# Performance work log

Measured on AMD Instinct MI355X. Metric: run time of the kernel, lower is better.

Reference implementation:

```python
import jax, jax.numpy as jnp
import numpy as np

B, T, DIM = 1, 2048, 2048
H, KV, D = 16, 4, 128
REP = H // KV
L, S = 32, 16          # cmp_len, cmp_stride
LP = 64                # slc_block
TOPK = 16
WIN = 512
CMP_HID = 2 * D
GATE_HID = DIM // 4
SCALE = D ** -0.5
TC = (T - L) // S + 1  # number of compressed blocks
NS = T // LP           # number of selection blocks
NEG = -1e30


def setup_inputs() -> dict:
    key = jax.random.key(0)
    ks = jax.random.split(key, 12)
    n = lambda k, sh: jax.random.normal(k, sh, jnp.float32) * 0.02
    return dict(
        x=jax.random.normal(ks[0], (B, T, DIM), jnp.float32),
        W_qkv=n(ks[1], ((H + 2 * KV) * D, DIM)), b_qkv=jnp.zeros(((H + 2 * KV) * D,), jnp.float32),
        W_out=n(ks[2], (DIM, H * D)), b_out=jnp.zeros((DIM,), jnp.float32),
        sinks=jnp.zeros((H,), jnp.float32),
        cmp_pos=n(ks[3], (L, D)),
        W_c1=n(ks[4], (CMP_HID, L * D)), b_c1=jnp.zeros((CMP_HID,), jnp.float32),
        W_c2=n(ks[5], (D, CMP_HID)), b_c2=jnp.zeros((D,), jnp.float32),
        W_g1=n(ks[6], (GATE_HID, DIM)), b_g1=jnp.zeros((GATE_HID,), jnp.float32),
        W_g2=n(ks[7], (3, GATE_HID)), b_g2=jnp.array([-2.2, -2.2, 1.4], jnp.float32),
    )


def _nsa(x, W_qkv, b_qkv, W_out, b_out, sinks, cmp_pos,
         W_c1, b_c1, W_c2, b_c2, W_g1, b_g1, W_g2, b_g2):
    qkv = x @ W_qkv.T + b_qkv
    q = qkv[..., :H * D].reshape(B, T, H, D)
    k = qkv[..., H * D:(H + KV) * D].reshape(B, T, KV, D)
    v = qkv[..., (H + KV) * D:].reshape(B, T, KV, D)

    t_idx = jnp.arange(T)
    # ---- compression phi over overlapping blocks (Eq 7) ----
    starts = jnp.arange(TC) * S
    gidx = starts[:, None] + jnp.arange(L)[None, :]          # [TC,L]

    def compress(z):                                          # [B,T,KV,D] -> [B,TC,KV,D]
        blk = z[:, gidx] + cmp_pos[None, None, :, None, :]    # [B,TC,L,KV,D]
        blk = blk.transpose(0, 1, 3, 2, 4).reshape(B, TC, KV, L * D)
        h = jax.nn.gelu(blk @ W_c1.T + b_c1, approximate=False)
        return h @ W_c2.T + b_c2

    k_cmp = jnp.repeat(compress(k), REP, axis=2)              # [B,TC,H,D]
    v_cmp = jnp.repeat(compress(v), REP, axis=2)

    # ---- CMP attention (Eq 8) ----
    c_logits = jnp.einsum('bthd,bchd->bhtc', q, k_cmp) * SCALE
    valid = (starts[None, :] + L - 1) <= t_idx[:, None]       # block fully in past [T,TC]
    c_logits = jnp.where(valid[None, None], c_logits, NEG)
    p = jax.nn.softmax(c_logits, axis=-1)
    any_valid = valid.any(axis=-1)                            # [T]
    p = jnp.where(any_valid[None, None, :, None], p, 0.0)
    o_cmp = jnp.einsum('bhtc,bchd->bthd', p, v_cmp)

    # ---- block score aggregation (Eq 9) + head sum (Eq 10) ----
    j_idx = jnp.arange(NS)
    ov = (starts[None, :] < (j_idx[:, None] + 1) * LP) & (starts[None, :] + L > j_idx[:, None] * LP)
    blk_scores = jnp.einsum('bhtc,jc->btj', p, ov.astype(p.dtype))  # [B,T,NS]
    cur_blk = t_idx // LP
    masked = jnp.where((j_idx[None, :] >= cur_blk[:, None])[None], -jnp.inf, blk_scores)
    _, dyn_idx = jax.lax.top_k(masked, TOPK - 3)              # Eq 11 (3 fixed blocks)
    fixed = jnp.stack([jnp.zeros_like(cur_blk), jnp.clip(cur_blk - 2, 0),
                       jnp.clip(cur_blk - 1, 0)], axis=-1)    # [T,3]
    all_blk = jnp.concatenate([jnp.broadcast_to(fixed[None], (B, T, 3)), dyn_idx], axis=-1)

    # ---- SLC sparse block attention (Eq 12) ----
    allowed = jax.nn.one_hot(all_blk, NS).sum(-2) > 0         # [B,T,NS]
    allowed = allowed | (j_idx[None, None, :] == cur_blk[None, :, None])  # own block dense
    tok_allowed = jnp.repeat(allowed, LP, axis=-1)            # [B,T,T]
    causal = t_idx[None, :] <= t_idx[:, None]                 # [T,T] (query, key)
    K = jnp.repeat(k, REP, axis=2)
    V = jnp.repeat(v, REP, axis=2)
    base = jnp.einsum('bthd,bshd->bhts', q, K) * SCALE        # shared logits
    s_logits = jnp.where((tok_allowed & causal[None])[:, None], base, NEG)
    o_slc = jnp.einsum('bhts,bshd->bthd', jax.nn.softmax(s_logits, -1), V)

    # ---- SWA sliding window with attention sinks ----
    swa_mask = causal & (t_idx[None, :] > t_idx[:, None] - WIN)
    w_logits = jnp.where(swa_mask[None, None], base, NEG)
    sink = jnp.broadcast_to(sinks[None, :, None, None], (B, H, T, 1))
    pw = jax.nn.softmax(jnp.concatenate([w_logits, sink], axis=-1), -1)[..., :T]
    o_swa = jnp.einsum('bhts,bshd->bthd', pw, V)

    # ---- sigmoid gating (Eq 5) + output proj ----
    g = jax.nn.sigmoid(jax.nn.gelu(x @ W_g1.T + b_g1, approximate=False) @ W_g2.T + b_g2)
    o = (g[..., 0, None, None] * o_cmp + g[..., 1, None, None] * o_slc
         + g[..., 2, None, None] * o_swa)                     # [B,T,H,D]
    return o.reshape(B, T, H * D) @ W_out.T + b_out


def reference(x, W_qkv, b_qkv, W_out, b_out, sinks, cmp_pos,
              W_c1, b_c1, W_c2, b_c2, W_g1, b_g1, W_g2, b_g2):
    return _nsa(x, W_qkv, b_qkv, W_out, b_out, sinks, cmp_pos,
                W_c1, b_c1, W_c2, b_c2, W_g1, b_g1, W_g2, b_g2)
```

## Files before the change

### kernel.cpp

```cpp
#include <hip/hip_runtime.h>
#include <hip/hip_bf16.h>

#define DEV static __device__ __forceinline__

constexpr int T_ = 2048, DIM_ = 2048, H_ = 16, KVH = 4, D_ = 128;
constexpr int LL = 32, SS = 16, TOPK_ = 16, WIN_ = 512;
constexpr int GATE_HID_ = 512;
constexpr int TC_ = 127, NS_ = 32;
constexpr int QKV_N = (H_ + 2 * KVH) * D_;
constexpr float SCALE_ = 0.08838834764831845f;

typedef __attribute__((ext_vector_type(8))) short short8;
typedef __attribute__((ext_vector_type(4))) float f32x4;
typedef __attribute__((ext_vector_type(4))) float float4v;
typedef __attribute__((ext_vector_type(4))) unsigned short u16x4;

DEV unsigned short f2b(float x) {
    return __builtin_bit_cast(unsigned short, __float2bfloat16(x));
}
DEV float b2f(unsigned short u) { return __builtin_bit_cast(float, ((unsigned)u) << 16); }
DEV float gelu_f(float x) { return 0.5f * x * (1.f + erff(x * 0.70710678118654752f)); }

DEV void g2l16(const void* g, void* l) {
    __builtin_amdgcn_global_load_lds((const __attribute__((address_space(1))) unsigned int*)g,
                                     (__attribute__((address_space(3))) unsigned int*)l, 16, 0, 0);
}

__global__ void cvt_f2b(const float* __restrict__ s, unsigned short* __restrict__ d, int n) {
    const int i = (blockIdx.x * 256 + threadIdx.x) * 4;
    if (i >= n) return;
    float4v v = *(const float4v*)(s + i);
    u16x4 o;
#pragma unroll
    for (int j = 0; j < 4; j++) o[j] = f2b(v[j]);
    *(u16x4*)(d + i) = o;
}

__global__ void cvt_all(const float* __restrict__ x, const float* __restrict__ wq,
                        const float* __restrict__ wg, const float* __restrict__ wc1,
                        const float* __restrict__ wc2,
                        unsigned short* __restrict__ xb, unsigned short* __restrict__ wqb,
                        unsigned short* __restrict__ wgb, unsigned short* __restrict__ wc1b,
                        unsigned short* __restrict__ wc2b) {
    const long i = ((long)blockIdx.x * 256 + threadIdx.x) * 4;
    const float* s;
    unsigned short* d;
    long off;
    if (i < 4194304)        { s = x;   d = xb;   off = i; }
    else if (i < 10485760)  { s = wq;  d = wqb;  off = i - 4194304; }
    else if (i < 11534336)  { s = wg;  d = wgb;  off = i - 10485760; }
    else if (i < 12582912)  { s = wc1; d = wc1b; off = i - 11534336; }
    else if (i < 12615680)  { s = wc2; d = wc2b; off = i - 12582912; }
    else return;
    float4v v = *(const float4v*)(s + off);
    u16x4 o;
#pragma unroll
    for (int j = 0; j < 4; j++) o[j] = f2b(v[j]);
    *(u16x4*)(d + off) = o;
}

DEV void stage64(const unsigned short* __restrict__ src, unsigned short* dstL,
                 int K, int tid) {
#pragma unroll
    for (int it = 0; it < 4; it++) {
        const int e = it * 256 + tid;
        const int row = e >> 3, cg = e & 7;
        g2l16(src + (size_t)row * K + ((cg ^ (row & 7)) << 3), dstL + e * 8);
    }
}
DEV short8 frag64(const unsigned short* Ls, int row, int g) {
    return *(const short8*)&Ls[row * 64 + ((g ^ (row & 7)) << 3)];
}

template <int ACT, bool WF, bool WB>
__global__ __launch_bounds__(256) void gemm_f(const unsigned short* __restrict__ A,
                                              const unsigned short* __restrict__ B,
                                              const float* __restrict__ bias,
                                              float* __restrict__ Cf,
                                              unsigned short* __restrict__ Cb,
                                              int M, int N, int K) {
    __shared__ __align__(16) unsigned short As[128 * 64];
    __shared__ __align__(16) unsigned short Bs[128 * 64];
    const int tid = threadIdx.x;
    const int w = tid >> 6, l = tid & 63;
    const int lc = l & 15, lg = l >> 4;
    const int wr = w >> 1, wc = w & 1;
    const int m0 = blockIdx.y * 128, n0 = blockIdx.x * 128;
    f32x4 acc[4][4] = {};
    for (int k0 = 0; k0 < K; k0 += 64) {
        stage64(A + (size_t)m0 * K + k0, As, K, tid);
        stage64(B + (size_t)n0 * K + k0, Bs, K, tid);
        __syncthreads();
#pragma unroll
        for (int ks = 0; ks < 2; ks++) {
            short8 af[4], bfr[4];
#pragma unroll
            for (int mi = 0; mi < 4; mi++) af[mi] = frag64(As, wr * 64 + mi * 16 + lc, ks * 4 + lg);
#pragma unroll
            for (int ni = 0; ni < 4; ni++) bfr[ni] = frag64(Bs, wc * 64 + ni * 16 + lc, ks * 4 + lg);
#pragma unroll
            for (int mi = 0; mi < 4; mi++)
#pragma unroll
                for (int ni = 0; ni < 4; ni++)
                    acc[mi][ni] = __builtin_amdgcn_mfma_f32_16x16x32_bf16(af[mi], bfr[ni], acc[mi][ni], 0, 0, 0);
        }
        __syncthreads();
    }
#pragma unroll
    for (int mi = 0; mi < 4; mi++) {
        const int gr = m0 + wr * 64 + mi * 16 + lg * 4;
#pragma unroll
        for (int ni = 0; ni < 4; ni++) {
            const int gc = n0 + wc * 64 + ni * 16 + lc;
            const float bv = bias[gc];
#pragma unroll
            for (int r = 0; r < 4; r++) {
                float v = acc[mi][ni][r] + bv;
                if (ACT == 1) v = gelu_f(v);
                const size_t idx = (size_t)(gr + r) * N + gc;
                if (WF) Cf[idx] = v;
                if (WB) Cb[idx] = f2b(v);
            }
        }
    }
}

__global__ __launch_bounds__(256) void gemm_qkvg(const unsigned short* __restrict__ A,
                                                 const unsigned short* __restrict__ Bq,
                                                 const unsigned short* __restrict__ Bg,
                                                 const float* __restrict__ bq,
                                                 const float* __restrict__ bg,
                                                 unsigned short* __restrict__ Cq,
                                                 float* __restrict__ Cg) {
    __shared__ __align__(16) unsigned short As[128 * 64];
    __shared__ __align__(16) unsigned short Bs[128 * 64];
    const int K = DIM_;
    const int tid = threadIdx.x;
    const int w = tid >> 6, l = tid & 63;
    const int lc = l & 15, lg = l >> 4;
    const int wr = w >> 1, wc = w & 1;
    const int m0 = blockIdx.y * 128, n0 = blockIdx.x * 128;
    const bool isg = (n0 >= QKV_N);
    const unsigned short* B = isg ? (Bg + (size_t)(n0 - QKV_N) * K) : (Bq + (size_t)n0 * K);
    f32x4 acc[4][4] = {};
    for (int k0 = 0; k0 < K; k0 += 64) {
        stage64(A + (size_t)m0 * K + k0, As, K, tid);
        stage64(B + k0, Bs, K, tid);
        __syncthreads();
#pragma unroll
        for (int ks = 0; ks < 2; ks++) {
            short8 af[4], bfr[4];
#pragma unroll
            for (int mi = 0; mi < 4; mi++) af[mi] = frag64(As, wr * 64 + mi * 16 + lc, ks * 4 + lg);
#pragma unroll
            for (int ni = 0; ni < 4; ni++) bfr[ni] = frag64(Bs, wc * 64 + ni * 16 + lc, ks * 4 + lg);
#pragma unroll
            for (int mi = 0; mi < 4; mi++)
#pragma unroll
                for (int ni = 0; ni < 4; ni++)
                    acc[mi][ni] = __builtin_amdgcn_mfma_f32_16x16x32_bf16(af[mi], bfr[ni], acc[mi][ni], 0, 0, 0);
        }
        __syncthreads();
    }
#pragma unroll
    for (int mi = 0; mi < 4; mi++) {
        const int gr = m0 + wr * 64 + mi * 16 + lg * 4;
#pragma unroll
        for (int ni = 0; ni < 4; ni++) {
            const int gcl = (n0 - (isg ? QKV_N : 0)) + wc * 64 + ni * 16 + lc;
            const float bv = isg ? bg[gcl] : bq[gcl];
#pragma unroll
            for (int r = 0; r < 4; r++) {
                const float v = acc[mi][ni][r] + bv;
                if (isg) Cg[(size_t)(gr + r) * GATE_HID_ + gcl] = gelu_f(v);
                else Cq[(size_t)(gr + r) * QKV_N + gcl] = f2b(v);
            }
        }
    }
}

__global__ __launch_bounds__(256) void gemm_c1p(const unsigned short* __restrict__ A,
                                                const unsigned short* __restrict__ B,
                                                float* __restrict__ part) {
    __shared__ __align__(16) unsigned short As[128 * 64];
    __shared__ __align__(16) unsigned short Bs[128 * 64];
    const int K = 4096, N = 256;
    const int tid = threadIdx.x;
    const int w = tid >> 6, l = tid & 63;
    const int lc = l & 15, lg = l >> 4;
    const int wr = w >> 1, wc = w & 1;
    const int m0 = blockIdx.y * 128, n0 = blockIdx.x * 128;
    const int kz = blockIdx.z * 1024;
    f32x4 acc[4][4] = {};
    for (int k0 = kz; k0 < kz + 1024; k0 += 64) {
        stage64(A + (size_t)m0 * K + k0, As, K, tid);
        stage64(B + (size_t)n0 * K + k0, Bs, K, tid);
        __syncthreads();
#pragma unroll
        for (int ks = 0; ks < 2; ks++) {
            short8 af[4], bfr[4];
#pragma unroll
            for (int mi = 0; mi < 4; mi++) af[mi] = frag64(As, wr * 64 + mi * 16 + lc, ks * 4 + lg);
#pragma unroll
            for (int ni = 0; ni < 4; ni++) bfr[ni] = frag64(Bs, wc * 64 + ni * 16 + lc, ks * 4 + lg);
#pragma unroll
            for (int mi = 0; mi < 4; mi++)
#pragma unroll
                for (int ni = 0; ni < 4; ni++)
                    acc[mi][ni] = __builtin_amdgcn_mfma_f32_16x16x32_bf16(af[mi], bfr[ni], acc[mi][ni], 0, 0, 0);
        }
        __syncthreads();
    }
    float* dst = part + (size_t)blockIdx.z * 2048 * 256;
#pragma unroll
    for (int mi = 0; mi < 4; mi++) {
        const int gr = m0 + wr * 64 + mi * 16 + lg * 4;
#pragma unroll
        for (int ni = 0; ni < 4; ni++) {
            const int gc = n0 + wc * 64 + ni * 16 + lc;
#pragma unroll
            for (int r = 0; r < 4; r++) dst[(size_t)(gr + r) * N + gc] = acc[mi][ni][r];
        }
    }
}

__global__ void c1_red(const float* __restrict__ part, const float* __restrict__ bias,
                       unsigned short* __restrict__ out) {
    const int i4 = blockIdx.x * 256 + threadIdx.x;
    const int base = i4 * 4;
    const int col = base & 255;
    float4v v = *(const float4v*)(part + base);
#pragma unroll
    for (int z = 1; z < 4; z++) {
        float4v p = *(const float4v*)(part + (size_t)z * 524288 + base);
#pragma unroll
        for (int j = 0; j < 4; j++) v[j] += p[j];
    }
    u16x4 o;
#pragma unroll
    for (int j = 0; j < 4; j++) o[j] = f2b(gelu_f(v[j] + bias[col + j]));
    *(u16x4*)(out + base) = o;
}

__global__ __launch_bounds__(256) void gemm_c2(const unsigned short* __restrict__ A,
                                               const unsigned short* __restrict__ B,
                                               const float* __restrict__ bias,
                                               unsigned short* __restrict__ Cb,
                                               unsigned short* __restrict__ vcmpT) {
    __shared__ __align__(16) unsigned short As[128 * 64];
    __shared__ __align__(16) unsigned short Bs[128 * 64];
    const int K = 256, N = 128;
    const int tid = threadIdx.x;
    const int w = tid >> 6, l = tid & 63;
    const int lc = l & 15, lg = l >> 4;
    const int wr = w >> 1, wc = w & 1;
    const int m0 = blockIdx.y * 128;
    f32x4 acc[4][4] = {};
    for (int k0 = 0; k0 < K; k0 += 64) {
        stage64(A + (size_t)m0 * K + k0, As, K, tid);
        stage64(B + k0, Bs, K, tid);
        __syncthreads();
#pragma unroll
        for (int ks = 0; ks < 2; ks++) {
            short8 af[4], bfr[4];
#pragma unroll
            for (int mi = 0; mi < 4; mi++) af[mi] = frag64(As, wr * 64 + mi * 16 + lc, ks * 4 + lg);
#pragma unroll
            for (int ni = 0; ni < 4; ni++) bfr[ni] = frag64(Bs, wc * 64 + ni * 16 + lc, ks * 4 + lg);
#pragma unroll
            for (int mi = 0; mi < 4; mi++)
#pragma unroll
                for (int ni = 0; ni < 4; ni++)
                    acc[mi][ni] = __builtin_amdgcn_mfma_f32_16x16x32_bf16(af[mi], bfr[ni], acc[mi][ni], 0, 0, 0);
        }
        __syncthreads();
    }
#pragma unroll
    for (int mi = 0; mi < 4; mi++) {
        const int gr = m0 + wr * 64 + mi * 16 + lg * 4;
#pragma unroll
        for (int ni = 0; ni < 4; ni++) {
            const int gc = wc * 64 + ni * 16 + lc;
            const float bv = bias[gc];
#pragma unroll
            for (int r = 0; r < 4; r++) {
                const int row = gr + r;
                const float v = acc[mi][ni][r] + bv;
                const unsigned short bv16 = f2b(v);
                Cb[(size_t)row * N + gc] = bv16;
                if (row >= 1024) {
                    const int mm = row - 1024;
                    const int cc = mm >> 2, kvv = mm & 3;
                    if (cc < 128) vcmpT[((size_t)(kvv * 128 + gc)) * 128 + cc] = bv16;
                }
            }
        }
    }
}

__global__ __launch_bounds__(256) void post_qkv(const unsigned short* __restrict__ qkvb,
                                                const float* __restrict__ cmp_pos,
                                                const float* __restrict__ hg,
                                                const float* __restrict__ Wg2,
                                                const float* __restrict__ bg2,
                                                unsigned short* __restrict__ kvTs,
                                                float* __restrict__ gate,
                                                unsigned short* __restrict__ blk) {
    const int bb = blockIdx.x;
    const int tid = threadIdx.x;
    if (bb < 128) {
        const int kv = bb & 3, tb = bb >> 2;
        const int t0 = tb * 64;
        unsigned short* dstK = kvTs + (size_t)(kv * 32 + tb) * 16384;
        unsigned short* dstV = dstK + 8192;
        const int kcol0 = H_ * D_ + kv * D_;
        const int vcol0 = H_ * D_ + KVH * D_ + kv * D_;
#pragma unroll
        for (int it = 0; it < 4; it++) {
            const int c = it * 256 + tid;
            const int key = c >> 4, g = c & 15;
            short8 v = *(const short8*)(qkvb + (size_t)(t0 + key) * QKV_N + kcol0 + g * 8);
            *(short8*)(dstK + key * 128 + ((g ^ (key & 7)) << 3)) = v;
        }
        __shared__ __align__(16) unsigned short tile[64][136];
        const int rr = tid >> 4, d0 = (tid & 15) * 8;
#pragma unroll
        for (int mIt = 0; mIt < 4; mIt++) {
            const int row = rr + mIt * 16;
            *(short8*)&tile[row][d0] = *(const short8*)(qkvb + (size_t)(t0 + row) * QKV_N + vcol0 + d0);
        }
        __syncthreads();
        const int d = tid >> 1, half = tid & 1;
        unsigned short* dv = dstV + d * 64;
#pragma unroll
        for (int c2 = 0; c2 < 4; c2++) {
            const int g = half * 4 + c2;
            short8 v;
#pragma unroll
            for (int j = 0; j < 8; j++) v[j] = tile[g * 8 + j][d];
            *(short8*)(dv + ((g ^ (d & 7)) << 3)) = v;
        }
    } else if (bb < 1664) {
        const int gi = (bb - 128) * 4 + (tid >> 6);
        const int t = gi / 3, i = gi % 3;
        const int l = tid & 63;
        const float* h = hg + (size_t)t * GATE_HID_;
        const float* w = Wg2 + (size_t)i * GATE_HID_;
        float s = 0.f;
#pragma unroll
        for (int j = 0; j < GATE_HID_ / 64; j++) s += h[l + j * 64] * w[l + j * 64];
#pragma unroll
        for (int o = 32; o > 0; o >>= 1) s += __shfl_xor(s, o);
        if (l == 0) gate[gi] = 1.f / (1.f + expf(-(s + bg2[i])));
    } else {
        const int b = bb - 1664;
        const int which = b >> 10, m = b & 1023;
        unsigned short* dst = blk + ((size_t)(which * 1024 + m)) * (LL * D_);
        if (m >= TC_ * KVH) {
            short8 z = {};
#pragma unroll
            for (int it = 0; it < 2; it++) *(short8*)(dst + (tid + it * 256) * 8) = z;
            return;
        }
        const int c = m >> 2, kv = m & 3;
        const int col0 = H_ * D_ + which * KVH * D_ + kv * D_;
#pragma unroll
        for (int it = 0; it < 2; it++) {
            const int g = tid + it * 256;
            const int lrow = g >> 4, d0 = (g & 15) * 8;
            short8 z = *(const short8*)(qkvb + (size_t)(c * SS + lrow) * QKV_N + col0 + d0);
            float4v p0 = *(const float4v*)(cmp_pos + lrow * 128 + d0);
            float4v p1 = *(const float4v*)(cmp_pos + lrow * 128 + d0 + 4);
            short8 o;
#pragma unroll
            for (int j = 0; j < 4; j++) o[j] = (short)f2b(b2f((unsigned short)z[j]) + p0[j]);
#pragma unroll
            for (int j = 0; j < 4; j++) o[4 + j] = (short)f2b(b2f((unsigned short)z[4 + j]) + p1[j]);
            *(short8*)(dst + g * 8) = o;
        }
    }
}

__global__ __launch_bounds__(256) void cmp_attn2(const unsigned short* __restrict__ qkvb,
                                                 const unsigned short* __restrict__ kcmpb,
                                                 const unsigned short* __restrict__ vcmpT,
                                                 const float* __restrict__ gate,
                                                 float* __restrict__ obuf,
                                                 float* __restrict__ scg) {
    const int bid = blockIdx.x;
    const int kv = bid & 3;
    const int tx = bid >> 2;
    const int tt = (tx & 1) ? (tx >> 1) : (127 - (tx >> 1));
    const int t0 = tt * 16;
    const int tid = threadIdx.x;
    const int w = tid >> 6, l = tid & 63;
    const int lc = l & 15, lg = l >> 4;
    const int h = kv * 4 + w;

    __shared__ float pbuf[4][16][132];

    short8 aq[4];
    {
        const unsigned short* qp = qkvb + (size_t)(t0 + lc) * QKV_N + h * D_ + lg * 8;
#pragma unroll
        for (int ks = 0; ks < 4; ks++) aq[ks] = *(const short8*)(qp + ks * 32);
    }

    f32x4 sfr[8] = {};
#pragma unroll
    for (int nj = 0; nj < 8; nj++) {
        const int c = nj * 16 + lc;
        const unsigned short* kp = kcmpb + ((size_t)(c * 4 + kv)) * D_ + lg * 8;
#pragma unroll
        for (int ks = 0; ks < 4; ks++) {
            short8 bf = *(const short8*)(kp + ks * 32);
            sfr[nj] = __builtin_amdgcn_mfma_f32_16x16x32_bf16(aq[ks], bf, sfr[nj], 0, 0, 0);
        }
    }

#pragma unroll
    for (int r = 0; r < 4; r++) {
        const int t = t0 + lg * 4 + r;
        const int nv = (t >= LL - 1) ? ((t - (LL - 1)) >> 4) + 1 : 0;
        float lv[8], mx = -1e30f;
#pragma unroll
        for (int nj = 0; nj < 8; nj++) {
            const int c = nj * 16 + lc;
            const float v = (c < nv) ? sfr[nj][r] * SCALE_ : -1e30f;
            lv[nj] = v;
            mx = fmaxf(mx, v);
        }
#pragma unroll
        for (int o = 1; o < 16; o <<= 1) mx = fmaxf(mx, __shfl_xor(mx, o));
        float s = 0.f, pe[8];
#pragma unroll
        for (int nj = 0; nj < 8; nj++) {
            const float e = (lv[nj] > -1e29f) ? __expf(lv[nj] - mx) : 0.f;
            pe[nj] = e;
            s += e;
        }
#pragma unroll
        for (int o = 1; o < 16; o <<= 1) s += __shfl_xor(s, o);
        const float inv = (s > 0.f) ? 1.f / s : 0.f;
#pragma unroll
        for (int nj = 0; nj < 8; nj++) sfr[nj][r] = pe[nj] * inv;
    }

#pragma unroll
    for (int nj = 0; nj < 8; nj++)
#pragma unroll
        for (int r = 0; r < 4; r++) pbuf[w][lg * 4 + r][nj * 16 + lc] = sfr[nj][r];

    __syncthreads();

    for (int idx = tid; idx < 16 * NS_; idx += 256) {
        const int lt = idx >> 5, j = idx & 31;
        int clo = 4 * j - 1;
        if (clo < 0) clo = 0;
        const int chi = 4 * j + 3;
        float s = 0.f;
        for (int c = clo; c <= chi; c++)
            s += pbuf[0][lt][c] + pbuf[1][lt][c] + pbuf[2][lt][c] + pbuf[3][lt][c];
        scg[((size_t)kv * T_ + (t0 + lt)) * NS_ + j] = s;
    }

    short8 pa[4];
#pragma unroll
    for (int ks = 0; ks < 4; ks++) {
        const float* pr = &pbuf[w][lc][ks * 32 + lg * 8];
        short8 t;
#pragma unroll
        for (int j = 0; j < 8; j++) t[j] = (short)f2b(pr[j]);
        pa[ks] = t;
    }
    f32x4 acc[8] = {};
#pragma unroll
    for (int nj = 0; nj < 8; nj++) {
        const int dd = nj * 16 + lc;
        const unsigned short* vp = vcmpT + ((size_t)(kv * 128 + dd)) * 128 + lg * 8;
#pragma unroll
        for (int ks = 0; ks < 4; ks++) {
            short8 bf = *(const short8*)(vp + ks * 32);
            acc[nj] = __builtin_amdgcn_mfma_f32_16x16x32_bf16(pa[ks], bf, acc[nj], 0, 0, 0);
        }
    }

#pragma unroll
    for (int r = 0; r < 4; r++) {
        const int t = t0 + lg * 4 + r;
        const float g0 = gate[t * 3 + 0];
#pragma unroll
        for (int nj = 0; nj < 8; nj++)
            obuf[(size_t)t * (H_ * D_) + h * D_ + nj * 16 + lc] = g0 * acc[nj][r];
    }
}

__global__ __launch_bounds__(256) void topk_k(const float* __restrict__ scg,
                                              unsigned int* __restrict__ amask) {
    const int t = blockIdx.x * 256 + threadIdx.x;
    if (t >= T_) return;
    float sc[NS_];
#pragma unroll
    for (int j = 0; j < NS_; j++)
        sc[j] = scg[((size_t)0 * T_ + t) * NS_ + j] + scg[((size_t)1 * T_ + t) * NS_ + j] +
                scg[((size_t)2 * T_ + t) * NS_ + j] + scg[((size_t)3 * T_ + t) * NS_ + j];
    const int cur = t >> 6;
    unsigned int chosen = 0;
    for (int it = 0; it < TOPK_ - 3; it++) {
        float best = 0.f;
        int bj = -1;
        for (int j = 0; j < NS_; j++) {
            if ((chosen >> j) & 1u) continue;
            const float v = (j >= cur) ? -INFINITY : sc[j];
            if (bj < 0 || v > best) { best = v; bj = j; }
        }
        chosen |= 1u << bj;
    }
    int f1 = cur - 2; if (f1 < 0) f1 = 0;
    int f2 = cur - 1; if (f2 < 0) f2 = 0;
    chosen |= 1u | (1u << f1) | (1u << f2) | (1u << cur);
    amask[t] = chosen;
}

DEV void write_P(unsigned short* PsW, const float p[4][4], int lc, int lg) {
#pragma unroll
    for (int kt = 0; kt < 4; kt++) {
        const int col = kt * 16 + lc;
#pragma unroll
        for (int rp = 0; rp < 4; rp += 2) {
            unsigned int pk;
            asm("v_cvt_pk_bf16_f32 %0, %1, %2" : "=v"(pk) : "v"(p[kt][rp]), "v"(p[kt][rp + 1]));
            const int row0 = lg * 4 + rp;
            const int row1 = row0 + 1;
            PsW[row0 * 64 + (col ^ ((row0 & 7) << 3))] = (unsigned short)(pk & 0xFFFFu);
            PsW[row1 * 64 + (col ^ ((row1 & 7) << 3))] = (unsigned short)(pk >> 16);
        }
    }
}

DEV void stageKV(const unsigned short* __restrict__ src, unsigned short* dst, int tid) {
#pragma unroll
    for (int it = 0; it < 8; it++) {
        const int c = it * 256 + tid;
        g2l16(src + c * 8, dst + c * 8);
    }
}

__global__ __launch_bounds__(256) void slc_swa_pt(const unsigned short* __restrict__ qkvb,
                                                  const unsigned short* __restrict__ kvTs,
                                                  const unsigned int* __restrict__ amask,
                                                  float* __restrict__ mlp,
                                                  unsigned short* __restrict__ accp) {
    const int bid = blockIdx.x;
    const int pr = bid >> 5;
    const int hs = bid & 31;
    const int h = hs >> 1, seg = hs & 1;
    const int kv = h >> 2;
    const int tid = threadIdx.x;
    const int w = tid >> 6, l = tid & 63;
    const int lc = l & 15, lg = l >> 4;

    __shared__ __align__(16) unsigned short KV[2][16384];
    __shared__ __align__(16) unsigned short Ps[4][1024];

    const short8 ones = {0x3F80, 0x3F80, 0x3F80, 0x3F80, 0x3F80, 0x3F80, 0x3F80, 0x3F80};

    for (int it2 = 0; it2 < 2; it2++) {
        const int qb = it2 ? pr : (31 - pr);
        const int t0 = qb * 64;
        const int cur = qb;

        const unsigned int aml = amask[t0 + l];
        unsigned int u64v = aml;
#pragma unroll
        for (int o = 1; o < 64; o <<= 1) u64v |= __shfl_xor(u64v, o);
        unsigned int u16g = aml;
#pragma unroll
        for (int o = 1; o < 16; o <<= 1) u16g |= __shfl_xor(u16g, o);
        const unsigned int uni16 = __shfl(u16g, w * 16);
        unsigned int amr[4];
        int tq[4];
#pragma unroll
        for (int r = 0; r < 4; r++) {
            const int rl = w * 16 + lg * 4 + r;
            tq[r] = t0 + rl;
            amr[r] = __shfl(aml, rl);
        }
        const int tmin_w = t0 + w * 16;
        const int tmax_w = tmin_w + 15;

        const unsigned int curm = (cur >= 31) ? 0xFFFFFFFFu : ((1u << (cur + 1)) - 1u);
        int sl = qb - 8; if (sl < 0) sl = 0;
        const unsigned int swab = curm & ~((1u << sl) - 1u);
        const unsigned int act = (u64v & curm) | swab;
        unsigned int actseg = 0;
        {
            int rank = 0;
            for (int jb = 0; jb <= cur; jb++)
                if ((act >> jb) & 1u) {
                    if ((rank & 1) == seg) actseg |= 1u << jb;
                    rank++;
                }
        }

        short8 aq[4];
        {
            const unsigned short* qp = qkvb + (size_t)(t0 + w * 16 + lc) * QKV_N + h * D_ + lg * 8;
#pragma unroll
            for (int ks = 0; ks < 4; ks++) aq[ks] = *(const short8*)(qp + ks * 32);
        }

        f32x4 acc_s[8] = {};
        f32x4 acc_w[8] = {};
        f32x4 ls4 = {}, lw4 = {};
        float m[4];
#pragma unroll
        for (int r = 0; r < 4; r++) m[r] = -1e30f;

        const unsigned short* kvbase = kvTs + (size_t)kv * 32 * 16384;

        unsigned int rem = actseg;
        if (rem) {
            int jb = __ffs(rem) - 1;
            rem &= rem - 1;
            stageKV(kvbase + (size_t)jb * 16384, KV[0], tid);
            __syncthreads();
            int buf = 0;
            while (true) {
                const int jn = rem ? (__ffs(rem) - 1) : -1;
                if (jn >= 0) {
                    rem &= rem - 1;
                    stageKV(kvbase + (size_t)jn * 16384, KV[buf ^ 1], tid);
                }
                const bool slc_w = (uni16 >> jb) & 1u;
                const bool swa_w = (jb * 64 + 63) > (tmin_w - WIN_);
                if (slc_w || swa_w) {
                    const unsigned short* Kb = KV[buf];
                    const unsigned short* Vb = KV[buf] + 8192;
                    f32x4 sfr[4] = {};
                    __builtin_amdgcn_s_setprio(1);
#pragma unroll
                    for (int kt = 0; kt < 4; kt++) {
                        const int key = kt * 16 + lc;
#pragma unroll
                        for (int ks = 0; ks < 4; ks++) {
                            short8 bf = *(const short8*)&Kb[key * 128 + (((ks * 4 + lg) ^ (key & 7)) << 3)];
                            sfr[kt] = __builtin_amdgcn_mfma_f32_16x16x32_bf16(aq[ks], bf, sfr[kt], 0, 0, 0);
                        }
                    }
                    __builtin_amdgcn_s_setprio(0);
                    float base[4][4];
#pragma unroll
                    for (int kt = 0; kt < 4; kt++)
#pragma unroll
                        for (int r = 0; r < 4; r++) base[kt][r] = sfr[kt][r] * SCALE_;

                    float lmax[4];
#pragma unroll
                    for (int r = 0; r < 4; r++)
                        lmax[r] = fmaxf(fmaxf(base[0][r], base[1][r]), fmaxf(base[2][r], base[3][r]));
                    bool need = false;
#pragma unroll
                    for (int r = 0; r < 4; r++) need |= (lmax[r] > m[r] + 8.f);
                    if (__any(need)) {
#pragma unroll
                        for (int r = 0; r < 4; r++) {
                            float rm = lmax[r];
#pragma unroll
                            for (int o = 1; o < 16; o <<= 1) rm = fmaxf(rm, __shfl_xor(rm, o));
                            const float mn = fmaxf(m[r], rm);
                            const float scf = __expf(m[r] - mn);
                            m[r] = mn;
#pragma unroll
                            for (int j = 0; j < 8; j++) { acc_s[j][r] *= scf; acc_w[j][r] *= scf; }
                            ls4[r] *= scf;
                            lw4[r] *= scf;
                        }
                    }
                    float e[4][4];
#pragma unroll
                    for (int kt = 0; kt < 4; kt++)
#pragma unroll
                        for (int r = 0; r < 4; r++) e[kt][r] = __expf(base[kt][r] - m[r]);

                    if (slc_w) {
                        float ps[4][4];
                        if (jb < cur) {
                            float mr[4];
#pragma unroll
                            for (int r = 0; r < 4; r++) mr[r] = (float)((amr[r] >> jb) & 1u);
#pragma unroll
                            for (int kt = 0; kt < 4; kt++)
#pragma unroll
                                for (int r = 0; r < 4; r++) ps[kt][r] = e[kt][r] * mr[r];
                        } else {
#pragma unroll
                            for (int kt = 0; kt < 4; kt++) {
                                const int kpos = jb * 64 + kt * 16 + lc;
#pragma unroll
                                for (int r = 0; r < 4; r++) {
                                    const bool ok = (kpos <= tq[r]) && ((amr[r] >> jb) & 1u);
                                    ps[kt][r] = ok ? e[kt][r] : 0.f;
                                }
                            }
                        }
                        write_P(Ps[w], ps, lc, lg);
                        __builtin_amdgcn_s_setprio(1);
#pragma unroll
                        for (int ks2 = 0; ks2 < 2; ks2++) {
                            short8 af = *(const short8*)&Ps[w][lc * 64 + ((ks2 * 32 + lg * 8) ^ ((lc & 7) << 3))];
                            ls4 = __builtin_amdgcn_mfma_f32_16x16x32_bf16(af, ones, ls4, 0, 0, 0);
#pragma unroll
                            for (int nj = 0; nj < 8; nj++) {
                                const int dd = nj * 16 + lc;
                                short8 bf = *(const short8*)&Vb[dd * 64 + (((ks2 * 4 + lg) ^ (dd & 7)) << 3)];
                                acc_s[nj] = __builtin_amdgcn_mfma_f32_16x16x32_bf16(af, bf, acc_s[nj], 0, 0, 0);
                            }
                        }
                        __builtin_amdgcn_s_setprio(0);
                    }
                    if (swa_w) {
                        const bool fullwin = (jb < cur) && (jb * 64 > tmax_w - WIN_);
                        if (fullwin) {
                            write_P(Ps[w], e, lc, lg);
                        } else {
                            float pw[4][4];
#pragma unroll
                            for (int kt = 0; kt < 4; kt++) {
                                const int kpos = jb * 64 + kt * 16 + lc;
#pragma unroll
                                for (int r = 0; r < 4; r++) {
                                    const bool ok = (kpos <= tq[r]) && (kpos > tq[r] - WIN_);
                                    pw[kt][r] = ok ? e[kt][r] : 0.f;
                                }
                            }
                            write_P(Ps[w], pw, lc, lg);
                        }
                        __builtin_amdgcn_s_setprio(1);
#pragma unroll
                        for (int ks2 = 0; ks2 < 2; ks2++) {
                            short8 af = *(const short8*)&Ps[w][lc * 64 + ((ks2 * 32 + lg * 8) ^ ((lc & 7) << 3))];
                            lw4 = __builtin_amdgcn_mfma_f32_16x16x32_bf16(af, ones, lw4, 0, 0, 0);
#pragma unroll
                            for (int nj = 0; nj < 8; nj++) {
                                const int dd = nj * 16 + lc;
                                short8 bf = *(const short8*)&Vb[dd * 64 + (((ks2 * 4 + lg) ^ (dd & 7)) << 3)];
                                acc_w[nj] = __builtin_amdgcn_mfma_f32_16x16x32_bf16(af, bf, acc_w[nj], 0, 0, 0);
                            }
                        }
                        __builtin_amdgcn_s_setprio(0);
                    }
                }
                __syncthreads();
                buf ^= 1;
                if (jn < 0) break;
                jb = jn;
            }
        }

        const size_t base2 = (size_t)(qb * 16 + h) * 2 + seg;
        if (lc == 0) {
#pragma unroll
            for (int r = 0; r < 4; r++) {
                const int row = w * 16 + lg * 4 + r;
                float4v v;
                v[0] = m[r]; v[1] = ls4[r]; v[2] = m[r]; v[3] = lw4[r];
                *(float4v*)&mlp[(base2 * 64 + row) * 4] = v;
            }
        }
#pragma unroll
        for (int st = 0; st < 2; st++) {
            const f32x4* A = st ? acc_w : acc_s;
#pragma unroll
            for (int nj = 0; nj < 8; nj++)
#pragma unroll
                for (int r = 0; r < 4; r++) {
                    const int row = w * 16 + lg * 4 + r;
                    accp[((base2 * 2 + st) * 64 + row) * 128 + nj * 16 + lc] = f2b(A[nj][r]);
                }
        }
    }
}

__global__ __launch_bounds__(256) void slc_comb(const float* __restrict__ obuf,
                                                const float* __restrict__ mlp,
                                                const unsigned short* __restrict__ accp,
                                                const float* __restrict__ gate,
                                                const float* __restrict__ sinks,
                                                unsigned short* __restrict__ obufb) {
    const int t = blockIdx.x;
    const int qb = t >> 6, row = t & 63;
    const int tid = threadIdx.x;
    const int d = tid & 127, half = tid >> 7;
    const float g1 = gate[t * 3 + 1], g2 = gate[t * 3 + 2];
#pragma unroll
    for (int hh = 0; hh < 8; hh++) {
        const int h = half * 8 + hh;
        const size_t base2 = (size_t)(qb * 16 + h) * 2;
        const float4v ml0 = *(const float4v*)&mlp[((base2 + 0) * 64 + row) * 4];
        const float4v ml1 = *(const float4v*)&mlp[((base2 + 1) * 64 + row) * 4];
        const float Ms = fmaxf(ml0[0], ml1[0]);
        const float e0 = __expf(ml0[0] - Ms), e1 = __expf(ml1[0] - Ms);
        const float ls = ml0[1] * e0 + ml1[1] * e1;
        const float a0 = b2f(accp[(((base2 + 0) * 2 + 0) * 64 + row) * 128 + d]);
        const float a1 = b2f(accp[(((base2 + 1) * 2 + 0) * 64 + row) * 128 + d]);
        const float os = (a0 * e0 + a1 * e1) / ls;
        const float snk = sinks[h];
        const float Mw = fmaxf(fmaxf(ml0[2], ml1[2]), snk);
        const float w0 = __expf(ml0[2] - Mw), w1 = __expf(ml1[2] - Mw);
        const float den = ml0[3] * w0 + ml1[3] * w1 + __expf(snk - Mw);
        const float b0 = b2f(accp[(((base2 + 0) * 2 + 1) * 64 + row) * 128 + d]);
        const float b1 = b2f(accp[(((base2 + 1) * 2 + 1) * 64 + row) * 128 + d]);
        const float ow = (b0 * w0 + b1 * w1) / den;
        const size_t idx = (size_t)t * (H_ * D_) + h * D_ + d;
        obufb[idx] = f2b(obuf[idx] + g1 * os + g2 * ow);
    }
}

extern "C" void kernel_launch(void* const* d_in, const int* in_sizes, int n_in,
                              void* d_out, int out_size, void* d_ws, size_t ws_size,
                              hipStream_t stream) {
    const float* x = (const float*)d_in[0];
    const float* W_qkv = (const float*)d_in[1];
    const float* b_qkv = (const float*)d_in[2];
    const float* W_out = (const float*)d_in[3];
    const float* b_out = (const float*)d_in[4];
    const float* sinks = (const float*)d_in[5];
    const float* cmp_pos = (const float*)d_in[6];
    const float* W_c1 = (const float*)d_in[7];
    const float* b_c1 = (const float*)d_in[8];
    const float* W_c2 = (const float*)d_in[9];
    const float* b_c2 = (const float*)d_in[10];
    const float* W_g1 = (const float*)d_in[11];
    const float* b_g1 = (const float*)d_in[12];
    const float* W_g2 = (const float*)d_in[13];
    const float* b_g2 = (const float*)d_in[14];

    char* ws = (char*)d_ws;
    unsigned short* qkvb = (unsigned short*)(ws + 0);
    unsigned short* obufb = (unsigned short*)(ws + 0);
    char* A0 = ws + 12582912;
    unsigned short* Wqkv_b = (unsigned short*)(A0);
    unsigned short* blkb = (unsigned short*)(A0);
    float* obuf = (float*)(A0);
    char* B0 = ws + 29360128;
    unsigned short* x_b = (unsigned short*)(B0);
    unsigned short* kvTs = (unsigned short*)(B0);
    float* gateb = (float*)(ws + 37748736);
    unsigned int* amaskb = (unsigned int*)(ws + 37773312);
    float* scg = (float*)(ws + 37781504);
    float* mlp = (float*)(ws + 38830080);
    unsigned short* accp = (unsigned short*)(ws + 39878656);
    unsigned short* Wg1_b = (unsigned short*)(ws + 39878656);
    unsigned short* Wc1_b = (unsigned short*)(ws + 41975808);
    unsigned short* Wc2_b = (unsigned short*)(ws + 44072960);
    float* hgate = (float*)(ws + 44138496);
    unsigned short* hc_b = (unsigned short*)(ws + 48332800);
    unsigned short* hcmpb = (unsigned short*)(ws + 49381376);
    unsigned short* vcmpT = (unsigned short*)(ws + 49905664);
    float* c1part = (float*)(ws + 50036736);
    unsigned short* Wout_b = (unsigned short*)(ws + 39878656);
    float* outf = (float*)d_out;

    cvt_all<<<dim3(12320), 256, 0, stream>>>(x, W_qkv, W_g1, W_c1, W_c2,
                                             x_b, Wqkv_b, Wg1_b, Wc1_b, Wc2_b);
    gemm_qkvg<<<dim3((QKV_N + GATE_HID_) / 128, T_ / 128), 256, 0, stream>>>(
        x_b, Wqkv_b, Wg1_b, b_qkv, b_g1, qkvb, hgate);
    post_qkv<<<dim3(3712), 256, 0, stream>>>(qkvb, cmp_pos, hgate, W_g2, b_g2,
                                             kvTs, gateb, blkb);
    gemm_c1p<<<dim3(2, 16, 4), 256, 0, stream>>>(blkb, Wc1_b, c1part);
    c1_red<<<dim3(512), 256, 0, stream>>>(c1part, b_c1, hc_b);
    gemm_c2<<<dim3(1, 16), 256, 0, stream>>>(hc_b, Wc2_b, b_c2, hcmpb, vcmpT);
    cmp_attn2<<<dim3(512), 256, 0, stream>>>(qkvb, hcmpb, vcmpT, gateb, obuf, scg);
    topk_k<<<dim3(T_ / 256), 256, 0, stream>>>(scg, amaskb);
    slc_swa_pt<<<dim3(512), 256, 0, stream>>>(qkvb, kvTs, amaskb, mlp, accp);
    slc_comb<<<dim3(T_), 256, 0, stream>>>(obuf, mlp, accp, gateb, sinks, obufb);
    cvt_f2b<<<dim3(4096), 256, 0, stream>>>(W_out, Wout_b, DIM_ * H_ * D_);
    gemm_f<0, true, false><<<dim3(DIM_ / 128, T_ / 128), 256, 0, stream>>>(
        obufb, Wout_b, b_out, outf, nullptr, T_, DIM_, H_ * D_);
}
```

Baseline: 314.0 us.

## Split slc_swa work across key halves and row halves, launch 4x more blocks

Reworks the selection/sliding-window attention kernel so that each block handles 32 query rows instead of two 64-row passes. The four waves split as two row tiles times two key halves of each KV block, and the two key halves' softmax partial states are merged through shared memory at the end. The KV double buffer becomes a single buffer, which cuts LDS use so four blocks can fit per CU under launch_bounds(256,4), and the grid grows from 512 to 2048 blocks. The aim is more parallelism and occupancy. In exchange the kernel loses the overlap from prefetching the next KV block, stages the same KV blocks more times in total, and pays for an extra cross-wave reduction.

```diff
diff --git a/kernel.cpp b/kernel.cpp
--- a/kernel.cpp
+++ b/kernel.cpp
@@ -522,263 +522,284 @@
     amask[t] = chosen;
 }
 
-DEV void write_P(unsigned short* PsW, const float p[4][4], int lc, int lg) {
-#pragma unroll
-    for (int kt = 0; kt < 4; kt++) {
+DEV void stageKV(const unsigned short* __restrict__ src, unsigned short* dst, int tid) {
+#pragma unroll
+    for (int it = 0; it < 8; it++) {
+        const int c = it * 256 + tid;
+        g2l16(src + c * 8, dst + c * 8);
+    }
+}
+
+DEV void write_P2(unsigned short* PsW, const float p[2][4], int lc, int lg) {
+#pragma unroll
+    for (int kt = 0; kt < 2; kt++) {
         const int col = kt * 16 + lc;
+        const int gsw = (((col >> 3)) << 3);
 #pragma unroll
         for (int rp = 0; rp < 4; rp += 2) {
             unsigned int pk;
             asm("v_cvt_pk_bf16_f32 %0, %1, %2" : "=v"(pk) : "v"(p[kt][rp]), "v"(p[kt][rp + 1]));
             const int row0 = lg * 4 + rp;
             const int row1 = row0 + 1;
-            PsW[row0 * 64 + (col ^ ((row0 & 7) << 3))] = (unsigned short)(pk & 0xFFFFu);
-            PsW[row1 * 64 + (col ^ ((row1 & 7) << 3))] = (unsigned short)(pk >> 16);
-        }
-    }
-}
-
-DEV void stageKV(const unsigned short* __restrict__ src, unsigned short* dst, int tid) {
-#pragma unroll
-    for (int it = 0; it < 8; it++) {
-        const int c = it * 256 + tid;
-        g2l16(src + c * 8, dst + c * 8);
-    }
-}
-
-__global__ __launch_bounds__(256) void slc_swa_pt(const unsigned short* __restrict__ qkvb,
-                                                  const unsigned short* __restrict__ kvTs,
-                                                  const unsigned int* __restrict__ amask,
-                                                  float* __restrict__ mlp,
-                                                  unsigned short* __restrict__ accp) {
+            const int c0 = ((((col >> 3) ^ (row0 & 3)) << 3) | (col & 7));
+            const int c1 = ((((col >> 3) ^ (row1 & 3)) << 3) | (col & 7));
+            PsW[row0 * 32 + c0] = (unsigned short)(pk & 0xFFFFu);
+            PsW[row1 * 32 + c1] = (unsigned short)(pk >> 16);
+        }
+    }
+}
+
+__global__ __launch_bounds__(256, 4) void slc_swa_pt(const unsigned short* __restrict__ qkvb,
+                                                     const unsigned short* __restrict__ kvTs,
+                                                     const unsigned int* __restrict__ amask,
+                                                     float* __restrict__ mlp,
+                                                     unsigned short* __restrict__ accp) {
     const int bid = blockIdx.x;
-    const int pr = bid >> 5;
-    const int hs = bid & 31;
-    const int h = hs >> 1, seg = hs & 1;
+    const int qb = 31 - (bid >> 6);
+    const int rest = bid & 63;
+    const int h = rest >> 2;
+    const int rh = (rest >> 1) & 1;
+    const int seg = rest & 1;
     const int kv = h >> 2;
     const int tid = threadIdx.x;
     const int w = tid >> 6, l = tid & 63;
     const int lc = l & 15, lg = l >> 4;
-
-    __shared__ __align__(16) unsigned short KV[2][16384];
-    __shared__ __align__(16) unsigned short Ps[4][1024];
+    const int rt = w & 1, kh = w >> 1;
+    const int cur = qb;
+    const int tbase = qb * 64 + rh * 32;
+
+    __shared__ __align__(16) unsigned short KV[16384];
+    __shared__ __align__(16) unsigned short Ps[4][512];
+    __shared__ float mml[2][16][4];
+
+    const unsigned int aml = amask[tbase + (l & 31)];
+    unsigned int u32v = aml;
+#pragma unroll
+    for (int o = 1; o < 64; o <<= 1) u32v |= __shfl_xor(u32v, o);
+    unsigned int um = (((l & 31) >> 4) == rt) ? aml : 0u;
+#pragma unroll
+    for (int o = 1; o < 64; o <<= 1) um |= __shfl_xor(um, o);
+    const unsigned int uni16 = um;
+    unsigned int amr[4];
+#pragma unroll
+    for (int r = 0; r < 4; r++) amr[r] = __shfl(aml, rt * 16 + lg * 4 + r);
+    const int tmin_w = tbase + rt * 16;
+    const int tmax_w = tmin_w + 15;
+
+    const unsigned int curm = (cur >= 31) ? 0xFFFFFFFFu : ((1u << (cur + 1)) - 1u);
+    int sl = qb - 8; if (sl < 0) sl = 0;
+    const unsigned int swab = curm & ~((1u << sl) - 1u);
+    const unsigned int act = (u32v & curm) | swab;
+    unsigned int actseg = 0;
+    {
+        int rank = 0;
+        for (int jb = 0; jb <= cur; jb++)
+            if ((act >> jb) & 1u) {
+                if ((rank & 1) == seg) actseg |= 1u << jb;
+                rank++;
+            }
+    }
+
+    short8 aq[4];
+    {
+        const unsigned short* qp = qkvb + (size_t)(tmin_w + lc) * QKV_N + h * D_ + lg * 8;
+#pragma unroll
+        for (int ks = 0; ks < 4; ks++) aq[ks] = *(const short8*)(qp + ks * 32);
+    }
 
     const short8 ones = {0x3F80, 0x3F80, 0x3F80, 0x3F80, 0x3F80, 0x3F80, 0x3F80, 0x3F80};
 
-    for (int it2 = 0; it2 < 2; it2++) {
-        const int qb = it2 ? pr : (31 - pr);
-        const int t0 = qb * 64;
-        const int cur = qb;
-
-        const unsigned int aml = amask[t0 + l];
-        unsigned int u64v = aml;
-#pragma unroll
-        for (int o = 1; o < 64; o <<= 1) u64v |= __shfl_xor(u64v, o);
-        unsigned int u16g = aml;
-#pragma unroll
-        for (int o = 1; o < 16; o <<= 1) u16g |= __shfl_xor(u16g, o);
-        const unsigned int uni16 = __shfl(u16g, w * 16);
-        unsigned int amr[4];
-        int tq[4];
-#pragma unroll
-        for (int r = 0; r < 4; r++) {
-            const int rl = w * 16 + lg * 4 + r;
-            tq[r] = t0 + rl;
-            amr[r] = __shfl(aml, rl);
-        }
-        const int tmin_w = t0 + w * 16;
-        const int tmax_w = tmin_w + 15;
-
-        const unsigned int curm = (cur >= 31) ? 0xFFFFFFFFu : ((1u << (cur + 1)) - 1u);
-        int sl = qb - 8; if (sl < 0) sl = 0;
-        const unsigned int swab = curm & ~((1u << sl) - 1u);
-        const unsigned int act = (u64v & curm) | swab;
-        unsigned int actseg = 0;
-        {
-            int rank = 0;
-            for (int jb = 0; jb <= cur; jb++)
-                if ((act >> jb) & 1u) {
-                    if ((rank & 1) == seg) actseg |= 1u << jb;
-                    rank++;
+    f32x4 acc_s[8] = {};
+    f32x4 acc_w[8] = {};
+    f32x4 ls4 = {}, lw4 = {};
+    float m[4];
+#pragma unroll
+    for (int r = 0; r < 4; r++) m[r] = -1e30f;
+
+    const unsigned short* kvbase = kvTs + (size_t)kv * 32 * 16384;
+
+    unsigned int rem = actseg;
+    while (rem) {
+        const int jb = __ffs(rem) - 1;
+        rem &= rem - 1;
+        stageKV(kvbase + (size_t)jb * 16384, KV, tid);
+        __syncthreads();
+        const bool slc_w = (uni16 >> jb) & 1u;
+        const bool swa_w = (jb * 64 + 63) > (tmin_w - WIN_);
+        if (slc_w || swa_w) {
+            const unsigned short* Kb = KV;
+            const unsigned short* Vb = KV + 8192;
+            f32x4 sfr[2] = {};
+            __builtin_amdgcn_s_setprio(1);
+#pragma unroll
+            for (int kt = 0; kt < 2; kt++) {
+                const int key = kh * 32 + kt * 16 + lc;
+#pragma unroll
+                for (int ks = 0; ks < 4; ks++) {
+                    short8 bf = *(const short8*)&Kb[key * 128 + (((ks * 4 + lg) ^ (key & 7)) << 3)];
+                    sfr[kt] = __builtin_amdgcn_mfma_f32_16x16x32_bf16(aq[ks], bf, sfr[kt], 0, 0, 0);
                 }
-        }
-
-        short8 aq[4];
-        {
-            const unsigned short* qp = qkvb + (size_t)(t0 + w * 16 + lc) * QKV_N + h * D_ + lg * 8;
-#pragma unroll
-            for (int ks = 0; ks < 4; ks++) aq[ks] = *(const short8*)(qp + ks * 32);
-        }
-
-        f32x4 acc_s[8] = {};
-        f32x4 acc_w[8] = {};
-        f32x4 ls4 = {}, lw4 = {};
-        float m[4];
-#pragma unroll
-        for (int r = 0; r < 4; r++) m[r] = -1e30f;
-
-        const unsigned short* kvbase = kvTs + (size_t)kv * 32 * 16384;
-
-        unsigned int rem = actseg;
-        if (rem) {
-            int jb = __ffs(rem) - 1;
-            rem &= rem - 1;
-            stageKV(kvbase + (size_t)jb * 16384, KV[0], tid);
-            __syncthreads();
-            int buf = 0;
-            while (true) {
-                const int jn = rem ? (__ffs(rem) - 1) : -1;
-                if (jn >= 0) {
-                    rem &= rem - 1;
-                    stageKV(kvbase + (size_t)jn * 16384, KV[buf ^ 1], tid);
+            }
+            __builtin_amdgcn_s_setprio(0);
+            float base[2][4];
+#pragma unroll
+            for (int kt = 0; kt < 2; kt++)
+#pragma unroll
+                for (int r = 0; r < 4; r++) base[kt][r] = sfr[kt][r] * SCALE_;
+
+            float lmax[4];
+#pragma unroll
+            for (int r = 0; r < 4; r++) lmax[r] = fmaxf(base[0][r], base[1][r]);
+            bool need = false;
+#pragma unroll
+            for (int r = 0; r < 4; r++) need |= (lmax[r] > m[r] + 8.f);
+            if (__any(need)) {
+#pragma unroll
+                for (int r = 0; r < 4; r++) {
+                    float rm = lmax[r];
+#pragma unroll
+                    for (int o = 1; o < 16; o <<= 1) rm = fmaxf(rm, __shfl_xor(rm, o));
+                    const float mn = fmaxf(m[r], rm);
+                    const float scf = __expf(m[r] - mn);
+                    m[r] = mn;
+#pragma unroll
+                    for (int j = 0; j < 8; j++) { acc_s[j][r] *= scf; acc_w[j][r] *= scf; }
+                    ls4[r] *= scf;
+                    lw4[r] *= scf;
                 }
-                const bool slc_w = (uni16 >> jb) & 1u;
-                const bool swa_w = (jb * 64 + 63) > (tmin_w - WIN_);
-                if (slc_w || swa_w) {
-                    const unsigned short* Kb = KV[buf];
-                    const unsigned short* Vb = KV[buf] + 8192;
-                    f32x4 sfr[4] = {};
-                    __builtin_amdgcn_s_setprio(1);
-#pragma unroll
-                    for (int kt = 0; kt < 4; kt++) {
-                        const int key = kt * 16 + lc;
-#pragma unroll
-                        for (int ks = 0; ks < 4; ks++) {
-                            short8 bf = *(const short8*)&Kb[key * 128 + (((ks * 4 + lg) ^ (key & 7)) << 3)];
-                            sfr[kt] = __builtin_amdgcn_mfma_f32_16x16x32_bf16(aq[ks], bf, sfr[kt], 0, 0, 0);
+            }
+            float e[2][4];
+#pragma unroll
+            for (int kt = 0; kt < 2; kt++)
+#pragma unroll
+                for (int r = 0; r < 4; r++) e[kt][r] = __expf(base[kt][r] - m[r]);
+
+            if (slc_w) {
+                float ps[2][4];
+                if (jb < cur) {
+                    float mr[4];
+#pragma unroll
+                    for (int r = 0; r < 4; r++) mr[r] = (float)((amr[r] >> jb) & 1u);
+#pragma unroll
+                    for (int kt = 0; kt < 2; kt++)
+#pragma unroll
+                        for (int r = 0; r < 4; r++) ps[kt][r] = e[kt][r] * mr[r];
+                } else {
+#pragma unroll
+                    for (int kt = 0; kt < 2; kt++) {
+                        const int kpos = jb * 64 + kh * 32 + kt * 16 + lc;
+#pragma unroll
+                        for (int r = 0; r < 4; r++) {
+                            const bool ok = (kpos <= tmin_w + lg * 4 + r) && ((amr[r] >> jb) & 1u);
+                            ps[kt][r] = ok ? e[kt][r] : 0.f;
                         }
                     }
-                    __builtin_amdgcn_s_setprio(0);
-                    float base[4][4];
-#pragma unroll
-                    for (int kt = 0; kt < 4; kt++)
-#pragma unroll
-                        for (int r = 0; r < 4; r++) base[kt][r] = sfr[kt][r] * SCALE_;
-
-                    float lmax[4];
-#pragma unroll
-                    for (int r = 0; r < 4; r++)
-                        lmax[r] = fmaxf(fmaxf(base[0][r], base[1][r]), fmaxf(base[2][r], base[3][r]));
-                    bool need = false;
-#pragma unroll
-                    for (int r = 0; r < 4; r++) need |= (lmax[r] > m[r] + 8.f);
-                    if (__any(need)) {
+                }
+                write_P2(Ps[w], ps, lc, lg);
+                __builtin_amdgcn_s_setprio(1);
+                {
+                    short8 af = *(const short8*)&Ps[w][lc * 32 + ((lg ^ (lc & 3)) << 3)];
+                    ls4 = __builtin_amdgcn_mfma_f32_16x16x32_bf16(af, ones, ls4, 0, 0, 0);
+#pragma unroll
+                    for (int nj = 0; nj < 8; nj++) {
+                        const int dd = nj * 16 + lc;
+                        short8 bf = *(const short8*)&Vb[dd * 64 + (((kh * 4 + lg) ^ (dd & 7)) << 3)];
+                        acc_s[nj] = __builtin_amdgcn_mfma_f32_16x16x32_bf16(af, bf, acc_s[nj], 0, 0, 0);
+                    }
+                }
+                __builtin_amdgcn_s_setprio(0);
+            }
+            if (swa_w) {
+                const bool fullwin = (jb < cur) && (jb * 64 > tmax_w - WIN_);
+                if (fullwin) {
+                    write_P2(Ps[w], e, lc, lg);
+                } else {
+                    float pw[2][4];
+#pragma unroll
+                    for (int kt = 0; kt < 2; kt++) {
+                        const int kpos = jb * 64 + kh * 32 + kt * 16 + lc;
 #pragma unroll
                         for (int r = 0; r < 4; r++) {
-                            float rm = lmax[r];
-#pragma unroll
-                            for (int o = 1; o < 16; o <<= 1) rm = fmaxf(rm, __shfl_xor(rm, o));
-                            const float mn = fmaxf(m[r], rm);
-                            const float scf = __expf(m[r] - mn);
-                            m[r] = mn;
-#pragma unroll
-                            for (int j = 0; j < 8; j++) { acc_s[j][r] *= scf; acc_w[j][r] *= scf; }
-                            ls4[r] *= scf;
-                            lw4[r] *= scf;
+                            const int tq = tmin_w + lg * 4 + r;
+                            const bool ok = (kpos <= tq) && (kpos > tq - WIN_);
+                            pw[kt][r] = ok ? e[kt][r] : 0.f;
                         }
                     }
-                    float e[4][4];
-#pragma unroll
-                    for (int kt = 0; kt < 4; kt++)
-#pragma unroll
-                        for (int r = 0; r < 4; r++) e[kt][r] = __expf(base[kt][r] - m[r]);
-
-                    if (slc_w) {
-                        float ps[4][4];
-                        if (jb < cur) {
-                            float mr[4];
-#pragma unroll
-                            for (int r = 0; r < 4; r++) mr[r] = (float)((amr[r] >> jb) & 1u);
-#pragma unroll
-                            for (int kt = 0; kt < 4; kt++)
-#pragma unroll
-                                for (int r = 0; r < 4; r++) ps[kt][r] = e[kt][r] * mr[r];
-                        } else {
-#pragma unroll
-                            for (int kt = 0; kt < 4; kt++) {
-                                const int kpos = jb * 64 + kt * 16 + lc;
-#pragma unroll
-                                for (int r = 0; r < 4; r++) {
-                                    const bool ok = (kpos <= tq[r]) && ((amr[r] >> jb) & 1u);
-                                    ps[kt][r] = ok ? e[kt][r] : 0.f;
-                                }
-                            }
-                        }
-                        write_P(Ps[w], ps, lc, lg);
-                        __builtin_amdgcn_s_setprio(1);
-#pragma unroll
-                        for (int ks2 = 0; ks2 < 2; ks2++) {
-                            short8 af = *(const short8*)&Ps[w][lc * 64 + ((ks2 * 32 + lg * 8) ^ ((lc & 7) << 3))];
-                            ls4 = __builtin_amdgcn_mfma_f32_16x16x32_bf16(af, ones, ls4, 0, 0, 0);
-#pragma unroll
-                            for (int nj = 0; nj < 8; nj++) {
-                                const int dd = nj * 16 + lc;
-                                short8 bf = *(const short8*)&Vb[dd * 64 + (((ks2 * 4 + lg) ^ (dd & 7)) << 3)];
-                                acc_s[nj] = __builtin_amdgcn_mfma_f32_16x16x32_bf16(af, bf, acc_s[nj], 0, 0, 0);
-                            }
-                        }
-                        __builtin_amdgcn_s_setprio(0);
-                    }
-                    if (swa_w) {
-                        const bool fullwin = (jb < cur) && (jb * 64 > tmax_w - WIN_);
-                        if (fullwin) {
-                            write_P(Ps[w], e, lc, lg);
-                        } else {
-                            float pw[4][4];
-#pragma unroll
-                            for (int kt = 0; kt < 4; kt++) {
-                                const int kpos = jb * 64 + kt * 16 + lc;
-#pragma unroll
-                                for (int r = 0; r < 4; r++) {
-                                    const bool ok = (kpos <= tq[r]) && (kpos > tq[r] - WIN_);
-                                    pw[kt][r] = ok ? e[kt][r] : 0.f;
-                                }
-                            }
-                            write_P(Ps[w], pw, lc, lg);
-                        }
-                        __builtin_amdgcn_s_setprio(1);
-#pragma unroll
-                        for (int ks2 = 0; ks2 < 2; ks2++) {
-                            short8 af = *(const short8*)&Ps[w][lc * 64 + ((ks2 * 32 + lg * 8) ^ ((lc & 7) << 3))];
-                            lw4 = __builtin_amdgcn_mfma_f32_16x16x32_bf16(af, ones, lw4, 0, 0, 0);
-#pragma unroll
-                            for (int nj = 0; nj < 8; nj++) {
-                                const int dd = nj * 16 + lc;
-                                short8 bf = *(const short8*)&Vb[dd * 64 + (((ks2 * 4 + lg) ^ (dd & 7)) << 3)];
-                                acc_w[nj] = __builtin_amdgcn_mfma_f32_16x16x32_bf16(af, bf, acc_w[nj], 0, 0, 0);
-                            }
-                        }
-                        __builtin_amdgcn_s_setprio(0);
+                    write_P2(Ps[w], pw, lc, lg);
+                }
+                __builtin_amdgcn_s_setprio(1);
+                {
+                    short8 af = *(const short8*)&Ps[w][lc * 32 + ((lg ^ (lc & 3)) << 3)];
+                    lw4 = __builtin_amdgcn_mfma_f32_16x16x32_bf16(af, ones, lw4, 0, 0, 0);
+#pragma unroll
+                    for (int nj = 0; nj < 8; nj++) {
+                        const int dd = nj * 16 + lc;
+                        short8 bf = *(const short8*)&Vb[dd * 64 + (((kh * 4 + lg) ^ (dd & 7)) << 3)];
+                        acc_w[nj] = __builtin_amdgcn_mfma_f32_16x16x32_bf16(af, bf, acc_w[nj], 0, 0, 0);
                     }
                 }
-                __syncthreads();
-                buf ^= 1;
-                if (jn < 0) break;
-                jb = jn;
-            }
-        }
-
+                __builtin_amdgcn_s_setprio(0);
+            }
+        }
+        __syncthreads();
+    }
+
+    __syncthreads();
+    float* macc = (float*)KV;
+    if (kh == 1) {
+        if (lc == 0) {
+#pragma unroll
+            for (int r = 0; r < 4; r++) {
+                mml[rt][lg * 4 + r][0] = m[r];
+                mml[rt][lg * 4 + r][1] = ls4[r];
+                mml[rt][lg * 4 + r][2] = lw4[r];
+            }
+        }
+#pragma unroll
+        for (int nj = 0; nj < 8; nj++)
+#pragma unroll
+            for (int r = 0; r < 4; r++) {
+                macc[((size_t)(rt * 2 + 0) * 16 + lg * 4 + r) * 128 + nj * 16 + lc] = acc_s[nj][r];
+                macc[((size_t)(rt * 2 + 1) * 16 + lg * 4 + r) * 128 + nj * 16 + lc] = acc_w[nj][r];
+            }
+    }
+    __syncthreads();
+    if (kh == 0) {
+        float e0[4], e1[4];
+#pragma unroll
+        for (int r = 0; r < 4; r++) {
+            const int row = lg * 4 + r;
+            const float m1 = mml[rt][row][0];
+            const float M = fmaxf(m[r], m1);
+            e0[r] = __expf(m[r] - M);
+            e1[r] = __expf(m1 - M);
+            m[r] = M;
+            ls4[r] = ls4[r] * e0[r] + mml[rt][row][1] * e1[r];
+            lw4[r] = lw4[r] * e0[r] + mml[rt][row][2] * e1[r];
+        }
         const size_t base2 = (size_t)(qb * 16 + h) * 2 + seg;
         if (lc == 0) {
 #pragma unroll
             for (int r = 0; r < 4; r++) {
-                const int row = w * 16 + lg * 4 + r;
+                const int row = rh * 32 + rt * 16 + lg * 4 + r;
                 float4v v;
                 v[0] = m[r]; v[1] = ls4[r]; v[2] = m[r]; v[3] = lw4[r];
                 *(float4v*)&mlp[(base2 * 64 + row) * 4] = v;
             }
         }
 #pragma unroll
-        for (int st = 0; st < 2; st++) {
-            const f32x4* A = st ? acc_w : acc_s;
-#pragma unroll
-            for (int nj = 0; nj < 8; nj++)
-#pragma unroll
-                for (int r = 0; r < 4; r++) {
-                    const int row = w * 16 + lg * 4 + r;
-                    accp[((base2 * 2 + st) * 64 + row) * 128 + nj * 16 + lc] = f2b(A[nj][r]);
-                }
-        }
+        for (int nj = 0; nj < 8; nj++)
+#pragma unroll
+            for (int r = 0; r < 4; r++) {
+                const int rloc = lg * 4 + r;
+                const int row = rh * 32 + rt * 16 + rloc;
+                const float vs = acc_s[nj][r] * e0[r] +
+                                 macc[((size_t)(rt * 2 + 0) * 16 + rloc) * 128 + nj * 16 + lc] * e1[r];
+                const float vw = acc_w[nj][r] * e0[r] +
+                                 macc[((size_t)(rt * 2 + 1) * 16 + rloc) * 128 + nj * 16 + lc] * e1[r];
+                accp[((base2 * 2 + 0) * 64 + row) * 128 + nj * 16 + lc] = f2b(vs);
+                accp[((base2 * 2 + 1) * 64 + row) * 128 + nj * 16 + lc] = f2b(vw);
+            }
     }
 }
 
@@ -873,7 +894,7 @@
     gemm_c2<<<dim3(1, 16), 256, 0, stream>>>(hc_b, Wc2_b, b_c2, hcmpb, vcmpT);
     cmp_attn2<<<dim3(512), 256, 0, stream>>>(qkvb, hcmpb, vcmpT, gateb, obuf, scg);
     topk_k<<<dim3(T_ / 256), 256, 0, stream>>>(scg, amaskb);
-    slc_swa_pt<<<dim3(512), 256, 0, stream>>>(qkvb, kvTs, amaskb, mlp, accp);
+    slc_swa_pt<<<dim3(2048), 256, 0, stream>>>(qkvb, kvTs, amaskb, mlp, accp);
     slc_comb<<<dim3(T_), 256, 0, stream>>>(obuf, mlp, accp, gateb, sinks, obufb);
     cvt_f2b<<<dim3(4096), 256, 0, stream>>>(W_out, Wout_b, DIM_ * H_ * D_);
     gemm_f<0, true, false><<<dim3(DIM_ / 128, T_ / 128), 256, 0, stream>>>(
```

Result: slower. 402.3 us (+28.1%).
